# Kernel optimization log

Hardware: AMD Instinct MI355X
Metric: run time of the kernel (lower is better)

The kernel has to match this reference:

```python
import jax, jax.numpy as jnp
import numpy as np

D_MODEL = 1024
N_HEADS = 16
HEAD_DIM = D_MODEL // N_HEADS
B, S = 2, 2048


def setup_inputs() -> dict:
    key = jax.random.key(0)
    ks = jax.random.split(key, 6)
    scale = 1.0 / np.sqrt(D_MODEL)
    inputs = jax.random.normal(ks[0], (B, S, D_MODEL), dtype=jnp.float32)
    # causal mask: 1.0 where attention is disallowed (strictly upper triangular)
    mask = jnp.triu(jnp.ones((S, S), dtype=jnp.float32), k=1)[None, None, :, :]
    mask = jnp.broadcast_to(mask, (B, 1, S, S))
    Wq = jax.random.normal(ks[1], (D_MODEL, D_MODEL), dtype=jnp.float32) * scale
    Wk = jax.random.normal(ks[2], (D_MODEL, D_MODEL), dtype=jnp.float32) * scale
    Wv = jax.random.normal(ks[3], (D_MODEL, D_MODEL), dtype=jnp.float32) * scale
    Wo = jax.random.normal(ks[4], (D_MODEL, D_MODEL), dtype=jnp.float32) * scale
    z = jnp.zeros((D_MODEL,), dtype=jnp.float32)
    return {"inputs": inputs, "mask": mask, "Wq": Wq, "bq": z, "Wk": Wk,
            "bk": z, "Wv": Wv, "bv": z, "Wo": Wo, "bo": z}


def _split_heads(x):
    b, s, _ = x.shape
    return x.reshape(b, s, N_HEADS, HEAD_DIM).transpose(0, 2, 1, 3)  # [B,H,S,Dh]


def reference(inputs, mask, Wq, bq, Wk, bk, Wv, bv, Wo, bo):
    q = _split_heads(inputs @ Wq + bq)
    k = _split_heads(inputs @ Wk + bk)
    v = _split_heads(inputs @ Wv + bv)
    # scaled dot-product attention with additive big-negative mask
    logits = jnp.einsum('bhqd,bhkd->bhqk', q, k) / jnp.sqrt(
        jnp.asarray(HEAD_DIM, dtype=q.dtype))
    logits = logits + mask * jnp.asarray(-1e9, dtype=q.dtype)
    attn_prob = jax.nn.softmax(logits, axis=-1)  # [B,H,S,S]
    ctx = jnp.einsum('bhqk,bhkd->bhqd', attn_prob, v)
    ctx = ctx.transpose(0, 2, 1, 3).reshape(inputs.shape[0], -1, D_MODEL)
    outputs = ctx @ Wo + bo
    return outputs, attn_prob
```

## Files before the change

### kernel.cpp

```cpp
#include <hip/hip_runtime.h>
#include <cstdint>

namespace {

typedef __attribute__((ext_vector_type(8))) short bf16x8;
typedef __attribute__((ext_vector_type(4))) short bf16x4;
typedef __attribute__((ext_vector_type(4))) float f32x4;

constexpr int D  = 1024;
constexpr int H  = 16;
constexpr int DH = 64;
constexpr int B  = 2;
constexpr int S  = 2048;
constexpr int M  = B * S;
constexpr float SCALE_Q = 0.125f * 1.4426950408889634f;

__device__ inline unsigned short f2bf(float f) {
    union { float f; uint32_t u; } v{f};
    return (unsigned short)((v.u + 0x7fffu + ((v.u >> 16) & 1u)) >> 16);
}

__device__ inline void gload16(const void* g, void* l) {
    __builtin_amdgcn_global_load_lds(
        (const __attribute__((address_space(1))) void*)g,
        (__attribute__((address_space(3))) void*)l, 16, 0, 0);
}

__global__ __launch_bounds__(256) void pack_x(const float* __restrict__ x,
                                              unsigned short* __restrict__ xb) {
    const int i = (blockIdx.x * 256 + threadIdx.x) * 8;
    float4 a = *reinterpret_cast<const float4*>(&x[i]);
    float4 b = *reinterpret_cast<const float4*>(&x[i + 4]);
    bf16x8 o;
    o[0] = f2bf(a.x); o[1] = f2bf(a.y); o[2] = f2bf(a.z); o[3] = f2bf(a.w);
    o[4] = f2bf(b.x); o[5] = f2bf(b.y); o[6] = f2bf(b.z); o[7] = f2bf(b.w);
    *reinterpret_cast<bf16x8*>(&xb[i]) = o;
}

__global__ __launch_bounds__(256) void transpose_w4(
    const float* __restrict__ W0, const float* __restrict__ W1,
    const float* __restrict__ W2, const float* __restrict__ W3,
    unsigned short* __restrict__ WtAll)
{
    __shared__ unsigned short T[64][72];
    const int z = blockIdx.z;
    const float* W = z == 0 ? W0 : (z == 1 ? W1 : (z == 2 ? W2 : W3));
    unsigned short* Wt = WtAll + (size_t)z * D * D;
    const int n0 = blockIdx.x * 64, k0 = blockIdx.y * 64;
    const int t = threadIdx.x;
    #pragma unroll
    for (int i = 0; i < 16; ++i) {
        int idx = i * 256 + t, r = idx >> 6, c = idx & 63;
        T[r][c] = f2bf(W[(size_t)(k0 + r) * D + n0 + c]);
    }
    __syncthreads();
    #pragma unroll
    for (int i = 0; i < 16; ++i) {
        int idx = i * 256 + t, r = idx >> 6, c = idx & 63;
        Wt[(size_t)(n0 + r) * D + k0 + c] = T[c][r];
    }
}

template <int MODE>
__global__ __launch_bounds__(256) void mfma_gemm(
    const unsigned short* __restrict__ A, const unsigned short* __restrict__ Bt,
    const float* __restrict__ b0, const float* __restrict__ b1,
    const float* __restrict__ b2,
    unsigned short* __restrict__ oQ, unsigned short* __restrict__ oK,
    unsigned short* __restrict__ oVt, float* __restrict__ oF)
{
    __shared__ __align__(16) unsigned short As[128 * 64];
    __shared__ __align__(16) unsigned short Bs[128 * 64];
    const int t = threadIdx.x;
    const int lane = t & 63, w = t >> 6;
    const int wr = w >> 1, wc = w & 1;
    const int lo = lane & 15, hi = lane >> 4;
    const int m0 = blockIdx.y * 128, n0 = blockIdx.x * 128;

    f32x4 acc[4][4] = {};

    for (int k0 = 0; k0 < D; k0 += 64) {
        #pragma unroll
        for (int i = 0; i < 4; ++i) {
            const int row = i * 32 + w * 8 + (lane >> 3);
            const int gcol = ((lane & 7) * 8) ^ ((row & 7) * 8);
            gload16(&A[(size_t)(m0 + row) * D + k0 + gcol], &As[i * 2048 + w * 512]);
            gload16(&Bt[(size_t)(n0 + row) * D + k0 + gcol], &Bs[i * 2048 + w * 512]);
        }
        __syncthreads();
        #pragma unroll
        for (int kk = 0; kk < 2; ++kk) {
            bf16x8 a[4], b[4];
            #pragma unroll
            for (int m = 0; m < 4; ++m) {
                const int row = wr * 64 + m * 16 + lo;
                a[m] = *reinterpret_cast<const bf16x8*>(
                    &As[row * 64 + ((kk * 32 + hi * 8) ^ ((row & 7) * 8))]);
            }
            #pragma unroll
            for (int n = 0; n < 4; ++n) {
                const int row = wc * 64 + n * 16 + lo;
                b[n] = *reinterpret_cast<const bf16x8*>(
                    &Bs[row * 64 + ((kk * 32 + hi * 8) ^ ((row & 7) * 8))]);
            }
            #pragma unroll
            for (int m = 0; m < 4; ++m)
                #pragma unroll
                for (int n = 0; n < 4; ++n)
                    acc[m][n] = __builtin_amdgcn_mfma_f32_16x16x32_bf16(a[m], b[n], acc[m][n], 0, 0, 0);
        }
        __syncthreads();
    }

    if (MODE == 0) {
        const int which = n0 >> 10;
        if (which == 2) {
            #pragma unroll
            for (int m = 0; m < 4; ++m) {
                const int row0 = m0 + wr * 64 + m * 16 + hi * 4;
                const int b_ = row0 >> 11, s_ = row0 & (S - 1);
                #pragma unroll
                for (int n = 0; n < 4; ++n) {
                    const int nn = (n0 + wc * 64 + n * 16 + lo) & 1023;
                    const int h_ = nn >> 6, dh = nn & 63;
                    const float bcol = b2[nn];
                    bf16x4 o;
                    #pragma unroll
                    for (int r = 0; r < 4; ++r) o[r] = (short)f2bf(acc[m][n][r] + bcol);
                    *reinterpret_cast<bf16x4*>(
                        &oVt[((size_t)(b_ * H + h_) * DH + dh) * S + s_]) = o;
                }
            }
        } else {
            const float* bs = which == 0 ? b0 : b1;
            unsigned short* op = which == 0 ? oQ : oK;
            const float scale = which == 0 ? SCALE_Q : 1.0f;
            #pragma unroll
            for (int m = 0; m < 4; ++m)
                #pragma unroll
                for (int n = 0; n < 4; ++n) {
                    const int nn = (n0 + wc * 64 + n * 16 + lo) & 1023;
                    const float bcol = bs[nn];
                    const int h_ = nn >> 6, dh = nn & 63;
                    #pragma unroll
                    for (int r = 0; r < 4; ++r) {
                        const int row = m0 + wr * 64 + m * 16 + hi * 4 + r;
                        const int b_ = row >> 11, s_ = row & (S - 1);
                        op[(((size_t)(b_ * H + h_) * S) + s_) * DH + dh] =
                            f2bf((acc[m][n][r] + bcol) * scale);
                    }
                }
        }
    } else {
        #pragma unroll
        for (int m = 0; m < 4; ++m)
            #pragma unroll
            for (int n = 0; n < 4; ++n) {
                const int col = n0 + wc * 64 + n * 16 + lo;
                const float bcol = b0[col];
                #pragma unroll
                for (int r = 0; r < 4; ++r) {
                    const int row = m0 + wr * 64 + m * 16 + hi * 4 + r;
                    oF[(size_t)row * D + col] = acc[m][n][r] + bcol;
                }
            }
    }
}

__global__ __launch_bounds__(256) void attn_fused(
    const unsigned short* __restrict__ Q, const unsigned short* __restrict__ K,
    const unsigned short* __restrict__ Vt, float* __restrict__ P,
    unsigned short* __restrict__ ctxb)
{
    __shared__ __align__(16) float Pf[2][4][32][68];
    const int bh = blockIdx.x;
    const int y = blockIdx.y;
    const int Qt = (y < 8) ? 15 - y : y - 8;
    const int t = threadIdx.x, lane = t & 63, w = t >> 6;
    const int lo = lane & 15, hi = lane >> 4;
    const int qw = Qt * 128 + w * 32;
    const int jt_w = (qw + 31) >> 6;
    const unsigned short* Qb = Q + (size_t)bh * S * DH;
    const unsigned short* Kb = K + (size_t)bh * S * DH;
    const unsigned short* Vb = Vt + (size_t)bh * DH * S;
    float* Pb = P + (size_t)bh * S * S;

    bf16x8 aq[2][2];
    #pragma unroll
    for (int g = 0; g < 2; ++g)
        #pragma unroll
        for (int kk = 0; kk < 2; ++kk)
            aq[g][kk] = *reinterpret_cast<const bf16x8*>(
                &Qb[(size_t)(qw + g * 16 + lo) * DH + kk * 32 + hi * 8]);

    float li[2][4];
    {
        float rsum[2][4] = {};
        for (int jt = 0; jt < jt_w; ++jt) {
            f32x4 acc[2][4] = {};
            #pragma unroll
            for (int kk = 0; kk < 2; ++kk)
                #pragma unroll
                for (int n = 0; n < 4; ++n) {
                    bf16x8 bk = *reinterpret_cast<const bf16x8*>(
                        &Kb[(size_t)(jt * 64 + n * 16 + lo) * DH + kk * 32 + hi * 8]);
                    #pragma unroll
                    for (int g = 0; g < 2; ++g)
                        acc[g][n] = __builtin_amdgcn_mfma_f32_16x16x32_bf16(aq[g][kk], bk, acc[g][n], 0, 0, 0);
                }
            #pragma unroll
            for (int g = 0; g < 2; ++g)
                #pragma unroll
                for (int n = 0; n < 4; ++n)
                    #pragma unroll
                    for (int r = 0; r < 4; ++r) rsum[g][r] += exp2f(acc[g][n][r]);
        }
        {
            f32x4 acc[2][4] = {};
            #pragma unroll
            for (int kk = 0; kk < 2; ++kk)
                #pragma unroll
                for (int n = 0; n < 4; ++n) {
                    bf16x8 bk = *reinterpret_cast<const bf16x8*>(
                        &Kb[(size_t)(jt_w * 64 + n * 16 + lo) * DH + kk * 32 + hi * 8]);
                    #pragma unroll
                    for (int g = 0; g < 2; ++g)
                        acc[g][n] = __builtin_amdgcn_mfma_f32_16x16x32_bf16(aq[g][kk], bk, acc[g][n], 0, 0, 0);
                }
            #pragma unroll
            for (int n = 0; n < 4; ++n) {
                const int j = jt_w * 64 + n * 16 + lo;
                #pragma unroll
                for (int g = 0; g < 2; ++g)
                    #pragma unroll
                    for (int r = 0; r < 4; ++r) {
                        const float e = exp2f(acc[g][n][r]);
                        rsum[g][r] += (j > qw + g * 16 + hi * 4 + r) ? 0.f : e;
                    }
            }
        }
        #pragma unroll
        for (int g = 0; g < 2; ++g)
            #pragma unroll
            for (int r = 0; r < 4; ++r) {
                #pragma unroll
                for (int off = 1; off < 16; off <<= 1)
                    rsum[g][r] += __shfl_xor(rsum[g][r], off);
                li[g][r] = 1.0f / rsum[g][r];
            }
    }

    f32x4 actx[2][4] = {};

    for (int jt = 0; jt <= jt_w; ++jt) {
        float (*pf)[68] = Pf[jt & 1][w];
        f32x4 acc[2][4] = {};
        #pragma unroll
        for (int kk = 0; kk < 2; ++kk)
            #pragma unroll
            for (int n = 0; n < 4; ++n) {
                bf16x8 bk = *reinterpret_cast<const bf16x8*>(
                    &Kb[(size_t)(jt * 64 + n * 16 + lo) * DH + kk * 32 + hi * 8]);
                #pragma unroll
                for (int g = 0; g < 2; ++g)
                    acc[g][n] = __builtin_amdgcn_mfma_f32_16x16x32_bf16(aq[g][kk], bk, acc[g][n], 0, 0, 0);
            }
        if (jt < jt_w) {
            #pragma unroll
            for (int g = 0; g < 2; ++g)
                #pragma unroll
                for (int n = 0; n < 4; ++n)
                    #pragma unroll
                    for (int r = 0; r < 4; ++r)
                        pf[g * 16 + hi * 4 + r][n * 16 + lo] = exp2f(acc[g][n][r]) * li[g][r];
        } else {
            #pragma unroll
            for (int n = 0; n < 4; ++n) {
                const int j = jt_w * 64 + n * 16 + lo;
                #pragma unroll
                for (int g = 0; g < 2; ++g)
                    #pragma unroll
                    for (int r = 0; r < 4; ++r) {
                        float p = exp2f(acc[g][n][r]) * li[g][r];
                        pf[g * 16 + hi * 4 + r][n * 16 + lo] =
                            (j > qw + g * 16 + hi * 4 + r) ? 0.f : p;
                    }
            }
        }
        #pragma unroll
        for (int i2 = 0; i2 < 8; ++i2) {
            const int row = i2 * 4 + hi;
            f32x4 v = *reinterpret_cast<const f32x4*>(&pf[row][lo * 4]);
            __builtin_nontemporal_store(
                v, reinterpret_cast<f32x4*>(&Pb[(size_t)(qw + row) * S + jt * 64 + lo * 4]));
        }
        #pragma unroll
        for (int kk = 0; kk < 2; ++kk) {
            bf16x8 pa[2];
            #pragma unroll
            for (int g = 0; g < 2; ++g) {
                const float* src = &pf[g * 16 + lo][kk * 32 + hi * 8];
                float4 f0 = *reinterpret_cast<const float4*>(src);
                float4 f1 = *reinterpret_cast<const float4*>(src + 4);
                pa[g][0] = f2bf(f0.x); pa[g][1] = f2bf(f0.y);
                pa[g][2] = f2bf(f0.z); pa[g][3] = f2bf(f0.w);
                pa[g][4] = f2bf(f1.x); pa[g][5] = f2bf(f1.y);
                pa[g][6] = f2bf(f1.z); pa[g][7] = f2bf(f1.w);
            }
            #pragma unroll
            for (int n2 = 0; n2 < 4; ++n2) {
                bf16x8 bv = *reinterpret_cast<const bf16x8*>(
                    &Vb[(size_t)(n2 * 16 + lo) * S + jt * 64 + kk * 32 + hi * 8]);
                #pragma unroll
                for (int g = 0; g < 2; ++g)
                    actx[g][n2] = __builtin_amdgcn_mfma_f32_16x16x32_bf16(pa[g], bv, actx[g][n2], 0, 0, 0);
            }
        }
    }

    const f32x4 z = {0.f, 0.f, 0.f, 0.f};
    for (int jt = jt_w + 1; jt < S / 64; ++jt)
        #pragma unroll
        for (int rr = 0; rr < 8; ++rr) {
            const int qrow = qw + rr * 4 + hi;
            __builtin_nontemporal_store(
                z, reinterpret_cast<f32x4*>(&Pb[(size_t)qrow * S + jt * 64 + lo * 4]));
        }

    const int b_ = bh >> 4, h_ = bh & 15;
    #pragma unroll
    for (int g = 0; g < 2; ++g)
        #pragma unroll
        for (int n2 = 0; n2 < 4; ++n2)
            #pragma unroll
            for (int r = 0; r < 4; ++r) {
                const int qg = qw + g * 16 + hi * 4 + r;
                ctxb[((size_t)(b_ * S + qg)) * D + h_ * 64 + n2 * 16 + lo] = f2bf(actx[g][n2][r]);
            }
}

}

extern "C" void kernel_launch(void* const* d_in, const int* in_sizes, int n_in,
                              void* d_out, int out_size, void* d_ws, size_t ws_size,
                              hipStream_t stream) {
    const float* x  = (const float*)d_in[0];
    const float* Wq = (const float*)d_in[2];
    const float* bq = (const float*)d_in[3];
    const float* Wk = (const float*)d_in[4];
    const float* bk = (const float*)d_in[5];
    const float* Wv = (const float*)d_in[6];
    const float* bv = (const float*)d_in[7];
    const float* Wo = (const float*)d_in[8];
    const float* bo = (const float*)d_in[9];

    float* out = (float*)d_out;
    float* P   = out + (size_t)M * D;

    char* ws = (char*)d_ws;
    const size_t MB = 1u << 20;
    unsigned short* xb    = (unsigned short*)(ws);
    unsigned short* WtAll = (unsigned short*)(ws + 8 * MB);
    unsigned short* Qb    = (unsigned short*)(ws + 16 * MB);
    unsigned short* Kb    = (unsigned short*)(ws + 24 * MB);
    unsigned short* Vtb   = (unsigned short*)(ws + 32 * MB);
    unsigned short* ctxb  = (unsigned short*)(ws + 40 * MB);

    const dim3 blk(256);

    pack_x<<<dim3(M * D / (256 * 8)), blk, 0, stream>>>(x, xb);
    transpose_w4<<<dim3(16, 16, 4), blk, 0, stream>>>(Wq, Wk, Wv, Wo, WtAll);

    mfma_gemm<0><<<dim3(24, M / 128), blk, 0, stream>>>(
        xb, WtAll, bq, bk, bv, Qb, Kb, Vtb, nullptr);

    attn_fused<<<dim3(B * H, 16), blk, 0, stream>>>(Qb, Kb, Vtb, P, ctxb);

    mfma_gemm<1><<<dim3(8, M / 128), blk, 0, stream>>>(
        ctxb, WtAll + (size_t)3 * D * D, bo, nullptr, nullptr,
        nullptr, nullptr, nullptr, out);
}
```

Baseline: 243.1 us.

## Split attention key tiles across waves per 32-row strip with LDS reductions

Each block now handles a single 32-query strip, and its four waves take interleaved key tiles instead of separate query rows. Row sums and context partials are combined across waves through LDS with barriers. The grid grows from 512 to 2048 blocks, which balances the causal triangle better, and launch bounds request four blocks per CU. Probabilities are staged in LDS as bf16 rather than fp32, which halves LDS traffic but means the fp32 P output is now rounded through bf16, a precision risk.

```diff
diff --git a/kernel.cpp b/kernel.cpp
--- a/kernel.cpp
+++ b/kernel.cpp
@@ -18,6 +18,12 @@
 __device__ inline unsigned short f2bf(float f) {
     union { float f; uint32_t u; } v{f};
     return (unsigned short)((v.u + 0x7fffu + ((v.u >> 16) & 1u)) >> 16);
+}
+
+__device__ inline float bf2f(unsigned short b) {
+    union { uint32_t u; float f; } v;
+    v.u = ((uint32_t)b) << 16;
+    return v.f;
 }
 
 __device__ inline void gload16(const void* g, void* l) {
@@ -167,23 +173,26 @@
     }
 }
 
-__global__ __launch_bounds__(256) void attn_fused(
+__global__ __launch_bounds__(256, 4) void attn_fused(
     const unsigned short* __restrict__ Q, const unsigned short* __restrict__ K,
     const unsigned short* __restrict__ Vt, float* __restrict__ P,
     unsigned short* __restrict__ ctxb)
 {
-    __shared__ __align__(16) float Pf[2][4][32][68];
-    const int bh = blockIdx.x;
-    const int y = blockIdx.y;
-    const int Qt = (y < 8) ? 15 - y : y - 8;
+    __shared__ __align__(16) char smem[36864 + 512];
+    const int strip = 63 - blockIdx.x;
+    const int bh = blockIdx.y;
     const int t = threadIdx.x, lane = t & 63, w = t >> 6;
     const int lo = lane & 15, hi = lane >> 4;
-    const int qw = Qt * 128 + w * 32;
-    const int jt_w = (qw + 31) >> 6;
+    const int qw = strip * 32;
+    const int jt_d = (qw + 31) >> 6;
     const unsigned short* Qb = Q + (size_t)bh * S * DH;
     const unsigned short* Kb = K + (size_t)bh * S * DH;
     const unsigned short* Vb = Vt + (size_t)bh * DH * S;
     float* Pb = P + (size_t)bh * S * S;
+    unsigned short (*pf0)[72] = reinterpret_cast<unsigned short(*)[72]>(smem + w * 9216);
+    unsigned short (*pf1)[72] = reinterpret_cast<unsigned short(*)[72]>(smem + w * 9216 + 4608);
+    float* Cmb = reinterpret_cast<float*>(smem);
+    float (*Rs)[4] = reinterpret_cast<float(*)[4]>(smem + 36864);
 
     bf16x8 aq[2][2];
     #pragma unroll
@@ -193,10 +202,9 @@
             aq[g][kk] = *reinterpret_cast<const bf16x8*>(
                 &Qb[(size_t)(qw + g * 16 + lo) * DH + kk * 32 + hi * 8]);
 
-    float li[2][4];
     {
         float rsum[2][4] = {};
-        for (int jt = 0; jt < jt_w; ++jt) {
+        for (int jt = w; jt <= jt_d; jt += 4) {
             f32x4 acc[2][4] = {};
             #pragma unroll
             for (int kk = 0; kk < 2; ++kk)
@@ -208,35 +216,25 @@
                     for (int g = 0; g < 2; ++g)
                         acc[g][n] = __builtin_amdgcn_mfma_f32_16x16x32_bf16(aq[g][kk], bk, acc[g][n], 0, 0, 0);
                 }
-            #pragma unroll
-            for (int g = 0; g < 2; ++g)
-                #pragma unroll
-                for (int n = 0; n < 4; ++n)
-                    #pragma unroll
-                    for (int r = 0; r < 4; ++r) rsum[g][r] += exp2f(acc[g][n][r]);
-        }
-        {
-            f32x4 acc[2][4] = {};
-            #pragma unroll
-            for (int kk = 0; kk < 2; ++kk)
+            if (jt < jt_d) {
+                #pragma unroll
+                for (int g = 0; g < 2; ++g)
+                    #pragma unroll
+                    for (int n = 0; n < 4; ++n)
+                        #pragma unroll
+                        for (int r = 0; r < 4; ++r) rsum[g][r] += exp2f(acc[g][n][r]);
+            } else {
                 #pragma unroll
                 for (int n = 0; n < 4; ++n) {
-                    bf16x8 bk = *reinterpret_cast<const bf16x8*>(
-                        &Kb[(size_t)(jt_w * 64 + n * 16 + lo) * DH + kk * 32 + hi * 8]);
+                    const int j = jt_d * 64 + n * 16 + lo;
                     #pragma unroll
                     for (int g = 0; g < 2; ++g)
-                        acc[g][n] = __builtin_amdgcn_mfma_f32_16x16x32_bf16(aq[g][kk], bk, acc[g][n], 0, 0, 0);
+                        #pragma unroll
+                        for (int r = 0; r < 4; ++r) {
+                            const float e = exp2f(acc[g][n][r]);
+                            rsum[g][r] += (j > qw + g * 16 + hi * 4 + r) ? 0.f : e;
+                        }
                 }
-            #pragma unroll
-            for (int n = 0; n < 4; ++n) {
-                const int j = jt_w * 64 + n * 16 + lo;
-                #pragma unroll
-                for (int g = 0; g < 2; ++g)
-                    #pragma unroll
-                    for (int r = 0; r < 4; ++r) {
-                        const float e = exp2f(acc[g][n][r]);
-                        rsum[g][r] += (j > qw + g * 16 + hi * 4 + r) ? 0.f : e;
-                    }
             }
         }
         #pragma unroll
@@ -246,14 +244,30 @@
                 #pragma unroll
                 for (int off = 1; off < 16; off <<= 1)
                     rsum[g][r] += __shfl_xor(rsum[g][r], off);
-                li[g][r] = 1.0f / rsum[g][r];
-            }
-    }
+            }
+        if (lo == 0) {
+            #pragma unroll
+            for (int g = 0; g < 2; ++g)
+                #pragma unroll
+                for (int r = 0; r < 4; ++r)
+                    Rs[g * 16 + hi * 4 + r][w] = rsum[g][r];
+        }
+    }
+    __syncthreads();
+
+    float li[2][4];
+    #pragma unroll
+    for (int g = 0; g < 2; ++g)
+        #pragma unroll
+        for (int r = 0; r < 4; ++r) {
+            f32x4 v = *reinterpret_cast<const f32x4*>(Rs[g * 16 + hi * 4 + r]);
+            li[g][r] = 1.0f / ((v[0] + v[1]) + (v[2] + v[3]));
+        }
 
     f32x4 actx[2][4] = {};
-
-    for (int jt = 0; jt <= jt_w; ++jt) {
-        float (*pf)[68] = Pf[jt & 1][w];
+    int nproc = 0;
+    for (int jt = w; jt <= jt_d; jt += 4, ++nproc) {
+        unsigned short (*pf)[72] = (nproc & 1) ? pf1 : pf0;
         f32x4 acc[2][4] = {};
         #pragma unroll
         for (int kk = 0; kk < 2; ++kk)
@@ -265,32 +279,36 @@
                 for (int g = 0; g < 2; ++g)
                     acc[g][n] = __builtin_amdgcn_mfma_f32_16x16x32_bf16(aq[g][kk], bk, acc[g][n], 0, 0, 0);
             }
-        if (jt < jt_w) {
+        if (jt < jt_d) {
             #pragma unroll
             for (int g = 0; g < 2; ++g)
                 #pragma unroll
                 for (int n = 0; n < 4; ++n)
                     #pragma unroll
                     for (int r = 0; r < 4; ++r)
-                        pf[g * 16 + hi * 4 + r][n * 16 + lo] = exp2f(acc[g][n][r]) * li[g][r];
+                        pf[g * 16 + hi * 4 + r][n * 16 + lo] =
+                            f2bf(exp2f(acc[g][n][r]) * li[g][r]);
         } else {
             #pragma unroll
             for (int n = 0; n < 4; ++n) {
-                const int j = jt_w * 64 + n * 16 + lo;
+                const int j = jt_d * 64 + n * 16 + lo;
                 #pragma unroll
                 for (int g = 0; g < 2; ++g)
                     #pragma unroll
                     for (int r = 0; r < 4; ++r) {
-                        float p = exp2f(acc[g][n][r]) * li[g][r];
+                        const float p = exp2f(acc[g][n][r]) * li[g][r];
                         pf[g * 16 + hi * 4 + r][n * 16 + lo] =
-                            (j > qw + g * 16 + hi * 4 + r) ? 0.f : p;
+                            (j > qw + g * 16 + hi * 4 + r) ? (unsigned short)0 : f2bf(p);
                     }
             }
         }
         #pragma unroll
         for (int i2 = 0; i2 < 8; ++i2) {
             const int row = i2 * 4 + hi;
-            f32x4 v = *reinterpret_cast<const f32x4*>(&pf[row][lo * 4]);
+            bf16x4 pv = *reinterpret_cast<const bf16x4*>(&pf[row][lo * 4]);
+            f32x4 v;
+            #pragma unroll
+            for (int r = 0; r < 4; ++r) v[r] = bf2f((unsigned short)pv[r]);
             __builtin_nontemporal_store(
                 v, reinterpret_cast<f32x4*>(&Pb[(size_t)(qw + row) * S + jt * 64 + lo * 4]));
         }
@@ -298,15 +316,8 @@
         for (int kk = 0; kk < 2; ++kk) {
             bf16x8 pa[2];
             #pragma unroll
-            for (int g = 0; g < 2; ++g) {
-                const float* src = &pf[g * 16 + lo][kk * 32 + hi * 8];
-                float4 f0 = *reinterpret_cast<const float4*>(src);
-                float4 f1 = *reinterpret_cast<const float4*>(src + 4);
-                pa[g][0] = f2bf(f0.x); pa[g][1] = f2bf(f0.y);
-                pa[g][2] = f2bf(f0.z); pa[g][3] = f2bf(f0.w);
-                pa[g][4] = f2bf(f1.x); pa[g][5] = f2bf(f1.y);
-                pa[g][6] = f2bf(f1.z); pa[g][7] = f2bf(f1.w);
-            }
+            for (int g = 0; g < 2; ++g)
+                pa[g] = *reinterpret_cast<const bf16x8*>(&pf[g * 16 + lo][kk * 32 + hi * 8]);
             #pragma unroll
             for (int n2 = 0; n2 < 4; ++n2) {
                 bf16x8 bv = *reinterpret_cast<const bf16x8*>(
@@ -319,24 +330,44 @@
     }
 
     const f32x4 z = {0.f, 0.f, 0.f, 0.f};
-    for (int jt = jt_w + 1; jt < S / 64; ++jt)
+    for (int jt = w; jt < S / 64; jt += 4) {
+        if (jt <= jt_d) continue;
         #pragma unroll
         for (int rr = 0; rr < 8; ++rr) {
             const int qrow = qw + rr * 4 + hi;
             __builtin_nontemporal_store(
                 z, reinterpret_cast<f32x4*>(&Pb[(size_t)qrow * S + jt * 64 + lo * 4]));
         }
-
-    const int b_ = bh >> 4, h_ = bh & 15;
+    }
+
+    __syncthreads();
+
     #pragma unroll
     for (int g = 0; g < 2; ++g)
         #pragma unroll
         for (int n2 = 0; n2 < 4; ++n2)
             #pragma unroll
-            for (int r = 0; r < 4; ++r) {
-                const int qg = qw + g * 16 + hi * 4 + r;
-                ctxb[((size_t)(b_ * S + qg)) * D + h_ * 64 + n2 * 16 + lo] = f2bf(actx[g][n2][r]);
-            }
+            for (int r = 0; r < 4; ++r)
+                Cmb[w * 2048 + (g * 16 + hi * 4 + r) * 64 + n2 * 16 + lo] = actx[g][n2][r];
+
+    __syncthreads();
+
+    {
+        const int idx = t * 8;
+        const int row = idx >> 6, col = idx & 63;
+        f32x4 s0 = {}, s1 = {};
+        #pragma unroll
+        for (int w4 = 0; w4 < 4; ++w4) {
+            s0 += *reinterpret_cast<const f32x4*>(&Cmb[w4 * 2048 + idx]);
+            s1 += *reinterpret_cast<const f32x4*>(&Cmb[w4 * 2048 + idx + 4]);
+        }
+        const int b_ = bh >> 4, h_ = bh & 15;
+        bf16x8 o;
+        o[0] = f2bf(s0[0]); o[1] = f2bf(s0[1]); o[2] = f2bf(s0[2]); o[3] = f2bf(s0[3]);
+        o[4] = f2bf(s1[0]); o[5] = f2bf(s1[1]); o[6] = f2bf(s1[2]); o[7] = f2bf(s1[3]);
+        *reinterpret_cast<bf16x8*>(
+            &ctxb[((size_t)(b_ * S + qw + row)) * D + h_ * 64 + col]) = o;
+    }
 }
 
 }
@@ -374,7 +405,7 @@
     mfma_gemm<0><<<dim3(24, M / 128), blk, 0, stream>>>(
         xb, WtAll, bq, bk, bv, Qb, Kb, Vtb, nullptr);
 
-    attn_fused<<<dim3(B * H, 16), blk, 0, stream>>>(Qb, Kb, Vtb, P, ctxb);
+    attn_fused<<<dim3(64, B * H), blk, 0, stream>>>(Qb, Kb, Vtb, P, ctxb);
 
     mfma_gemm<1><<<dim3(8, M / 128), blk, 0, stream>>>(
         ctxb, WtAll + (size_t)3 * D * D, bo, nullptr, nullptr,
```

Result: slower. 319.5 us (+31.4%).
